# Kernel tuning notes

Measured on AMD Instinct MI355X. Metric: run time of the kernel, lower is better.

Reference implementation:

```python
import jax, jax.numpy as jnp
import numpy as np

B, S, D_MODEL, H = 2, 2048, 768, 12
HD = D_MODEL // H  # head_dim = 64
EPS = 1e-5


def setup_inputs() -> dict:
    key = jax.random.key(0)
    ks = jax.random.split(key, 5)
    sc = 0.02
    return {
        "x": jax.random.normal(ks[0], (B, S, D_MODEL), dtype=jnp.float32),
        "Wproj_w": jax.random.normal(ks[1], (7 * D_MODEL, D_MODEL), dtype=jnp.float32) * sc,
        "Wproj_b": jax.random.normal(ks[2], (7 * D_MODEL,), dtype=jnp.float32) * sc,
        "gn_w": jnp.ones((D_MODEL,), dtype=jnp.float32),
        "gn_b": jnp.zeros((D_MODEL,), dtype=jnp.float32),
        "out_w": jax.random.normal(ks[3], (D_MODEL, D_MODEL), dtype=jnp.float32) * sc,
        "out_b": jax.random.normal(ks[4], (D_MODEL,), dtype=jnp.float32) * sc,
    }


def _time_swiglu(qkv):
    # qkv: [B, S, 7, H, D]
    q1, k1, q2, k2, q3, k3, v = [qkv[:, :, i] for i in range(7)]
    a1 = jnp.einsum('bthd,bshd->bhts', q1, k1)  # [B,H,S,S], raw scores, no softmax
    a2 = jnp.einsum('bthd,bshd->bhts', q2, k2)
    a3 = jnp.einsum('bthd,bshd->bhts', q3, k3)
    t1 = jax.nn.silu(jnp.einsum('bhts,bshd->bthd', a1, v))
    t2 = jnp.einsum('bhts,bshd->bthd', a2, v)
    return jnp.einsum('bhts,bshd->bthd', a3, t1 * t2)  # [B,S,H,D]


def _group_norm(ctx, gn_w, gn_b):
    # ctx: [B, S, D_MODEL]; torch applies GroupNorm(H, D_MODEL) over (B, C=D_MODEL, L=S)
    g = ctx.reshape(B, S, H, HD)
    mean = jnp.mean(g, axis=(1, 3), keepdims=True)          # per (batch, group) over (S, HD)
    var = jnp.var(g, axis=(1, 3), keepdims=True)
    g = (g - mean) * jax.lax.rsqrt(var + EPS)
    g = g.reshape(B, S, D_MODEL)
    return g * gn_w + gn_b


def reference(x, Wproj_w, Wproj_b, gn_w, gn_b, out_w, out_b):
    qkv = x @ Wproj_w.T + Wproj_b                  # [B,S,7*D_MODEL]
    qkv = qkv.reshape(B, S, 7, H, HD)
    ctx = _time_swiglu(qkv).reshape(B, S, D_MODEL)  # [B,S,D_MODEL]
    ctx = _group_norm(ctx, gn_w, gn_b)
    return ctx @ out_w.T + out_b
```

## Files before the change

kernel.cpp:

```cpp
#include <hip/hip_runtime.h>
#include <hip/hip_bf16.h>
#include <stdint.h>

typedef short short8 __attribute__((ext_vector_type(8)));
typedef float f32x4 __attribute__((ext_vector_type(4)));
typedef float f32x16 __attribute__((ext_vector_type(16)));
typedef unsigned short u16x4 __attribute__((ext_vector_type(4)));
typedef unsigned uint4v __attribute__((ext_vector_type(4)));

#define MFMA16 __builtin_amdgcn_mfma_f32_16x16x32_bf16
#define MFMA32 __builtin_amdgcn_mfma_f32_32x32x16_bf16

typedef unsigned int __attribute__((address_space(1))) as1_u32;
typedef unsigned int __attribute__((address_space(3))) as3_u32;
#define GLOAD16(gsrc, ldst) \
  __builtin_amdgcn_global_load_lds((const as1_u32*)(gsrc), (as3_u32*)(ldst), 16, 0, 0)

__device__ __forceinline__ unsigned short f2bf(float f) {
  __hip_bfloat16 h = __float2bfloat16(f);
  return *(unsigned short*)&h;
}
__device__ __forceinline__ unsigned pk2(float lo, float hi) {
  return ((unsigned)f2bf(hi) << 16) | (unsigned)f2bf(lo);
}
__device__ __forceinline__ void plswap(unsigned &a, unsigned &b) {
  asm volatile("v_permlane32_swap_b32 %0, %1" : "+v"(a), "+v"(b));
}

__device__ __forceinline__ short8 pv_frag(const f32x16* acc, int kc2) {
  int n = kc2 >> 1, c = kc2 & 1;
  int o0 = 2 * c, o1 = 2 * c + 1;
  unsigned x0 = pk2(acc[n][o0 * 4 + 0], acc[n][o0 * 4 + 1]);
  unsigned x1 = pk2(acc[n][o0 * 4 + 2], acc[n][o0 * 4 + 3]);
  unsigned y0 = pk2(acc[n][o1 * 4 + 0], acc[n][o1 * 4 + 1]);
  unsigned y1 = pk2(acc[n][o1 * 4 + 2], acc[n][o1 * 4 + 3]);
  plswap(x0, y0);
  plswap(x1, y1);
  uint4v fu; fu.x = x0; fu.y = x1; fu.z = y0; fu.w = y1;
  return __builtin_bit_cast(short8, fu);
}

__global__ __launch_bounds__(256) void cvt_bf16_4(const float* __restrict__ in,
                                                  unsigned short* __restrict__ out,
                                                  int n) {
  int i = (blockIdx.x * 256 + threadIdx.x) * 4;
  if (i >= n) return;
  f32x4 v = *(const f32x4*)(in + i);
  u16x4 o;
  o.x = f2bf(v.x); o.y = f2bf(v.y); o.z = f2bf(v.z); o.w = f2bf(v.w);
  *(u16x4*)(out + i) = o;
}

__global__ __launch_bounds__(256) void transp64(const unsigned short* __restrict__ src,
                                                int stride, int off,
                                                unsigned short* __restrict__ dst) {
  __shared__ __align__(16) unsigned short t[64 * 64];
  const int tid = threadIdx.x;
  const int tt = blockIdx.x, bh = blockIdx.y;
  const int b = bh / 12, h = bh % 12;
  const unsigned short* sbase = src + (size_t)(b * 2048 + tt * 64) * stride + h * 64 + off;
  for (int it = 0; it < 2; ++it) {
    int slot = it * 256 + tid, s = slot >> 3, j = slot & 7;
    short8 v = *(const short8*)(sbase + (size_t)s * stride + j * 8);
    int phys = (s + 8 * j) & 63;
    for (int e = 0; e < 8; ++e)
      t[(j * 8 + e) * 64 + phys] = ((unsigned short*)&v)[e];
  }
  __syncthreads();
  unsigned short* dbase = dst + (size_t)bh * 64 * 2048 + tt * 64;
  for (int it = 0; it < 2; ++it) {
    int slot = it * 256 + tid, d = slot >> 3, c = slot & 7;
    int pc = (c + (d >> 3)) & 7;
    short8 v = *(const short8*)(t + d * 64 + pc * 8);
    *(short8*)(dbase + (size_t)d * 2048 + c * 8) = v;
  }
}

template <bool OUT_BF16>
__global__ __launch_bounds__(256) void gemm_nt(const unsigned short* __restrict__ A,
                                               const unsigned short* __restrict__ Bm,
                                               const float* __restrict__ bias,
                                               void* __restrict__ Cout,
                                               int M, int N, int K) {
  __shared__ __align__(16) char smem[32768];
  char* As = smem;
  char* Bs = smem + 16384;
  const int tid = threadIdx.x;
  const int w = tid >> 6, l = tid & 63;
  const int wm = w >> 1, wn = w & 1;
  const int gx = gridDim.x;
  const int lin = blockIdx.y * gx + blockIdx.x;
  const int cpx = (gx * gridDim.y) >> 3;
  const int swz = (lin & 7) * cpx + (lin >> 3);
  const int Row0 = (swz / gx) * 128, Col0 = (swz % gx) * 128;

  f32x4 z; z.x = 0.f; z.y = 0.f; z.z = 0.f; z.w = 0.f;
  f32x4 acc[4][4];
  for (int m = 0; m < 4; ++m)
    for (int n = 0; n < 4; ++n) acc[m][n] = z;

  for (int k0 = 0; k0 < K; k0 += 64) {
    for (int it = 0; it < 4; ++it) {
      int slot = it * 256 + tid;
      int row = slot >> 3, j = slot & 7;
      int gc = j ^ (row & 7);
      GLOAD16(A + (size_t)(Row0 + row) * K + k0 + gc * 8, As + slot * 16);
      GLOAD16(Bm + (size_t)(Col0 + row) * K + k0 + gc * 8, Bs + slot * 16);
    }
    __syncthreads();
    for (int kc = 0; kc < 2; ++kc) {
      int c = (l >> 4) + 4 * kc;
      short8 af[4], bf[4];
      for (int m = 0; m < 4; ++m) {
        int t = wm * 64 + m * 16 + (l & 15);
        af[m] = *(const short8*)(As + t * 128 + ((c ^ (t & 7)) * 16));
      }
      for (int n = 0; n < 4; ++n) {
        int t = wn * 64 + n * 16 + (l & 15);
        bf[n] = *(const short8*)(Bs + t * 128 + ((c ^ (t & 7)) * 16));
      }
      for (int m = 0; m < 4; ++m)
        for (int n = 0; n < 4; ++n)
          acc[m][n] = MFMA16(af[m], bf[n], acc[m][n], 0, 0, 0);
    }
    __syncthreads();
  }
  for (int n = 0; n < 4; ++n) {
    int col = Col0 + wn * 64 + n * 16 + (l & 15);
    float bv = bias[col];
    for (int m = 0; m < 4; ++m) {
      int rbase = Row0 + wm * 64 + m * 16 + (l >> 4) * 4;
      for (int r = 0; r < 4; ++r) {
        float v = acc[m][n][r] + bv;
        size_t idx = (size_t)(rbase + r) * N + col;
        if (OUT_BF16) ((unsigned short*)Cout)[idx] = f2bf(v);
        else          ((float*)Cout)[idx] = v;
      }
    }
  }
}

__global__ __launch_bounds__(256) void pass1(const unsigned short* __restrict__ qkv,
                                             const unsigned short* __restrict__ vt,
                                             unsigned short* __restrict__ u) {
  __shared__ __align__(16) char smem[49152];
  const int tid = threadIdx.x, w = tid >> 6, l = tid & 63;
  const int m = w & 1, sh = w >> 1;
  const int g5 = l >> 5, l31 = l & 31;
  const int tt = blockIdx.x, bh = blockIdx.y;
  const int b = bh / 12, h = bh % 12;

  short8 qf[2][4];
#pragma unroll
  for (int tb = 0; tb < 2; ++tb) {
    const unsigned short* qrow =
        qkv + (size_t)(b * 2048 + tt * 64 + tb * 32 + l31) * 5376 + h * 64 + m * 2 * 768;
#pragma unroll
    for (int kc = 0; kc < 4; ++kc)
      qf[tb][kc] = *(const short8*)(qrow + kc * 16 + g5 * 8);
  }

  f32x16 z16;
#pragma unroll
  for (int i = 0; i < 16; ++i) z16[i] = 0.f;
  f32x16 tacc[2][2];
  tacc[0][0] = z16; tacc[0][1] = z16; tacc[1][0] = z16; tacc[1][1] = z16;

  auto STAGE = [&](char* buf, int si) {
#pragma unroll
    for (int shs = 0; shs < 2; ++shs) {
      int s0 = shs * 1024 + si * 32;
      char* hb = buf + shs * 12288;
      {
        int row = tid >> 3, pc = tid & 7, gc = pc ^ (row & 7);
        const unsigned short* base =
            qkv + (size_t)(b * 2048 + s0 + row) * 5376 + h * 64 + gc * 8;
        GLOAD16(base + 768, hb + tid * 16);
        GLOAD16(base + 3 * 768, hb + 4096 + tid * 16);
      }
      {
        int row = tid >> 2, pc = tid & 3, gc = pc ^ ((row >> 1) & 3);
        GLOAD16(vt + (size_t)(bh * 64 + row) * 2048 + s0 + gc * 8,
                hb + 8192 + tid * 16);
      }
    }
  };

  STAGE(smem, 0);
  __syncthreads();
  for (int si = 0; si < 32; ++si) {
    const char* cur = smem + (si & 1) * 24576 + sh * 12288;
    if (si < 31) STAGE(smem + ((si + 1) & 1) * 24576, si + 1);
    const char* Ks = cur + m * 4096;
    const char* Vs = cur + 8192;

    short8 kreg[4], vreg[4];
#pragma unroll
    for (int kc = 0; kc < 4; ++kc)
      kreg[kc] = *(const short8*)(Ks + l31 * 128 + (((kc * 2 + g5) ^ (l31 & 7)) * 16));
#pragma unroll
    for (int kc2 = 0; kc2 < 2; ++kc2)
#pragma unroll
      for (int dn = 0; dn < 2; ++dn) {
        int drow = dn * 32 + l31, c = kc2 * 2 + g5;
        vreg[kc2 * 2 + dn] =
            *(const short8*)(Vs + drow * 64 + ((c ^ ((drow >> 1) & 3)) * 16));
      }

#pragma unroll
    for (int tb = 0; tb < 2; ++tb) {
      f32x16 a = z16;
#pragma unroll
      for (int kc = 0; kc < 4; ++kc)
        a = MFMA32(kreg[kc], qf[tb][kc], a, 0, 0, 0);
#pragma unroll
      for (int kc2 = 0; kc2 < 2; ++kc2) {
        short8 pa = pv_frag(&a, kc2);
#pragma unroll
        for (int dn = 0; dn < 2; ++dn)
          tacc[tb][dn] = MFMA32(pa, vreg[kc2 * 2 + dn], tacc[tb][dn], 0, 0, 0);
      }
    }
    __syncthreads();
  }

  float* ex = (float*)smem;
  if (sh == 1) {
#pragma unroll
    for (int tb = 0; tb < 2; ++tb)
#pragma unroll
      for (int dn = 0; dn < 2; ++dn)
#pragma unroll
        for (int qd = 0; qd < 4; ++qd) {
          f32x4 v;
          v.x = tacc[tb][dn][qd * 4 + 0]; v.y = tacc[tb][dn][qd * 4 + 1];
          v.z = tacc[tb][dn][qd * 4 + 2]; v.w = tacc[tb][dn][qd * 4 + 3];
          *(f32x4*)((char*)ex + m * 16384 + ((tb * 2 + dn) * 4 + qd) * 1024 + l * 16) = v;
        }
  }
  __syncthreads();
  if (sh == 0) {
#pragma unroll
    for (int tb = 0; tb < 2; ++tb)
#pragma unroll
      for (int dn = 0; dn < 2; ++dn)
#pragma unroll
        for (int qd = 0; qd < 4; ++qd) {
          f32x4 v = *(const f32x4*)((char*)ex + m * 16384 +
                                    ((tb * 2 + dn) * 4 + qd) * 1024 + l * 16);
          tacc[tb][dn][qd * 4 + 0] += v.x; tacc[tb][dn][qd * 4 + 1] += v.y;
          tacc[tb][dn][qd * 4 + 2] += v.z; tacc[tb][dn][qd * 4 + 3] += v.w;
        }
  }
  __syncthreads();
  if (sh == 0 && m == 1) {
#pragma unroll
    for (int tb = 0; tb < 2; ++tb)
#pragma unroll
      for (int dn = 0; dn < 2; ++dn)
#pragma unroll
        for (int qd = 0; qd < 4; ++qd) {
          f32x4 v;
          v.x = tacc[tb][dn][qd * 4 + 0]; v.y = tacc[tb][dn][qd * 4 + 1];
          v.z = tacc[tb][dn][qd * 4 + 2]; v.w = tacc[tb][dn][qd * 4 + 3];
          *(f32x4*)((char*)ex + ((tb * 2 + dn) * 4 + qd) * 1024 + l * 16) = v;
        }
  }
  __syncthreads();
  if (sh == 0 && m == 0) {
#pragma unroll
    for (int tb = 0; tb < 2; ++tb)
#pragma unroll
      for (int dn = 0; dn < 2; ++dn)
#pragma unroll
        for (int r = 0; r < 16; ++r) {
          float x2 = ex[((tb * 2 + dn) * 4 + (r >> 2)) * 256 + l * 4 + (r & 3)];
          int crow = (r & 3) + 8 * (r >> 2) + 4 * g5;
          int t = tt * 64 + tb * 32 + crow;
          int d = dn * 32 + l31;
          float x1 = tacc[tb][dn][r];
          float uu = (x1 / (1.f + expf(-x1))) * x2;
          u[(size_t)(b * 2048 + t) * 768 + h * 64 + d] = f2bf(uu);
        }
  }
}

__global__ __launch_bounds__(256) void pass2(const unsigned short* __restrict__ qkv,
                                             const unsigned short* __restrict__ ut,
                                             float* __restrict__ ctx,
                                             float* __restrict__ partials) {
  __shared__ __align__(16) char smem[65536];
  const int tid = threadIdx.x, w = tid >> 6, l = tid & 63;
  const int g5 = l >> 5, l31 = l & 31;
  const int tt = blockIdx.x, bh = blockIdx.y;
  const int b = bh / 12, h = bh % 12;

  short8 qf[2][4];
#pragma unroll
  for (int tb = 0; tb < 2; ++tb) {
    const unsigned short* qrow =
        qkv + (size_t)(b * 2048 + tt * 64 + tb * 32 + l31) * 5376 + h * 64 + 4 * 768;
#pragma unroll
    for (int kc = 0; kc < 4; ++kc)
      qf[tb][kc] = *(const short8*)(qrow + kc * 16 + g5 * 8);
  }

  f32x16 z16;
#pragma unroll
  for (int i = 0; i < 16; ++i) z16[i] = 0.f;
  f32x16 ca[2][2];
  ca[0][0] = z16; ca[0][1] = z16; ca[1][0] = z16; ca[1][1] = z16;

  const unsigned short *kp0, *kp1, *kp2, *kp3, *up0, *up1, *up2, *up3;
  {
    int row = tid >> 3, pc = tid & 7, gc = pc ^ (row & 7);
    kp0 = qkv + (size_t)(b * 2048 + row) * 5376 + h * 64 + 5 * 768 + gc * 8;
    kp1 = kp0 + (size_t)512 * 5376;
    kp2 = kp1 + (size_t)512 * 5376;
    kp3 = kp2 + (size_t)512 * 5376;
    int rowv = tid >> 2, pcv = tid & 3, gcv = pcv ^ ((rowv >> 1) & 3);
    up0 = ut + (size_t)(bh * 64 + rowv) * 2048 + gcv * 8;
    up1 = up0 + 512; up2 = up1 + 512; up3 = up2 + 512;
  }
  auto STAGE = [&](char* buf) {
    GLOAD16(kp0, buf + tid * 16);
    GLOAD16(up0, buf + 4096 + tid * 16);
    GLOAD16(kp1, buf + 8192 + tid * 16);
    GLOAD16(up1, buf + 12288 + tid * 16);
    GLOAD16(kp2, buf + 16384 + tid * 16);
    GLOAD16(up2, buf + 20480 + tid * 16);
    GLOAD16(kp3, buf + 24576 + tid * 16);
    GLOAD16(up3, buf + 28672 + tid * 16);
    kp0 += 32 * 5376; kp1 += 32 * 5376; kp2 += 32 * 5376; kp3 += 32 * 5376;
    up0 += 32; up1 += 32; up2 += 32; up3 += 32;
  };

  STAGE(smem);
  __syncthreads();
  for (int si = 0; si < 16; ++si) {
    const char* cur = smem + (si & 1) * 32768;
    if (si < 15) STAGE(smem + ((si + 1) & 1) * 32768);
    const char* Ks = cur + w * 8192;
    const char* Us = Ks + 4096;

    short8 kreg[4], ureg[4];
#pragma unroll
    for (int kc = 0; kc < 4; ++kc)
      kreg[kc] = *(const short8*)(Ks + l31 * 128 + (((kc * 2 + g5) ^ (l31 & 7)) * 16));
#pragma unroll
    for (int kc2 = 0; kc2 < 2; ++kc2)
#pragma unroll
      for (int dn = 0; dn < 2; ++dn) {
        int drow = dn * 32 + l31, c = kc2 * 2 + g5;
        ureg[kc2 * 2 + dn] =
            *(const short8*)(Us + drow * 64 + ((c ^ ((drow >> 1) & 3)) * 16));
      }

#pragma unroll
    for (int tb = 0; tb < 2; ++tb) {
      f32x16 a = z16;
#pragma unroll
      for (int kc = 0; kc < 4; ++kc)
        a = MFMA32(kreg[kc], qf[tb][kc], a, 0, 0, 0);
#pragma unroll
      for (int kc2 = 0; kc2 < 2; ++kc2) {
        short8 pa = pv_frag(&a, kc2);
#pragma unroll
        for (int dn = 0; dn < 2; ++dn)
          ca[tb][dn] = MFMA32(pa, ureg[kc2 * 2 + dn], ca[tb][dn], 0, 0, 0);
      }
    }
    __syncthreads();
  }

  float* ex = (float*)smem;
  auto DUMP = [&](int region) {
#pragma unroll
    for (int tb = 0; tb < 2; ++tb)
#pragma unroll
      for (int dn = 0; dn < 2; ++dn)
#pragma unroll
        for (int qd = 0; qd < 4; ++qd) {
          f32x4 v;
          v.x = ca[tb][dn][qd * 4 + 0]; v.y = ca[tb][dn][qd * 4 + 1];
          v.z = ca[tb][dn][qd * 4 + 2]; v.w = ca[tb][dn][qd * 4 + 3];
          *(f32x4*)((char*)ex + region * 16384 + ((tb * 2 + dn) * 4 + qd) * 1024 + l * 16) = v;
        }
  };
  auto ACCUM = [&](int region) {
#pragma unroll
    for (int tb = 0; tb < 2; ++tb)
#pragma unroll
      for (int dn = 0; dn < 2; ++dn)
#pragma unroll
        for (int qd = 0; qd < 4; ++qd) {
          f32x4 v = *(const f32x4*)((char*)ex + region * 16384 +
                                    ((tb * 2 + dn) * 4 + qd) * 1024 + l * 16);
          ca[tb][dn][qd * 4 + 0] += v.x; ca[tb][dn][qd * 4 + 1] += v.y;
          ca[tb][dn][qd * 4 + 2] += v.z; ca[tb][dn][qd * 4 + 3] += v.w;
        }
  };
  if (w == 1) DUMP(0);
  if (w == 3) DUMP(1);
  __syncthreads();
  if (w == 0) ACCUM(0);
  if (w == 2) ACCUM(1);
  __syncthreads();
  if (w == 2) DUMP(0);
  __syncthreads();
  float psum = 0.f, psum2 = 0.f;
  if (w == 0) {
    ACCUM(0);
#pragma unroll
    for (int tb = 0; tb < 2; ++tb)
#pragma unroll
      for (int dn = 0; dn < 2; ++dn)
#pragma unroll
        for (int r = 0; r < 16; ++r) {
          int t = tt * 64 + tb * 32 + (r & 3) + 8 * (r >> 2) + 4 * g5;
          int d = dn * 32 + l31;
          float v = ca[tb][dn][r];
          ctx[(size_t)(b * 2048 + t) * 768 + h * 64 + d] = v;
          psum += v; psum2 += v * v;
        }
    for (int off = 32; off > 0; off >>= 1) {
      psum += __shfl_down(psum, off, 64);
      psum2 += __shfl_down(psum2, off, 64);
    }
    if (l == 0) {
      partials[(bh * 32 + tt) * 2] = psum;
      partials[(bh * 32 + tt) * 2 + 1] = psum2;
    }
  }
}

__global__ __launch_bounds__(64) void gn_finalize(const float* __restrict__ partials,
                                                  float* __restrict__ stats) {
  const int g = blockIdx.x;
  const int l = threadIdx.x;
  double s = 0.0, s2 = 0.0;
  if (l < 32) {
    s = (double)partials[(g * 32 + l) * 2];
    s2 = (double)partials[(g * 32 + l) * 2 + 1];
  }
  for (int off = 32; off > 0; off >>= 1) {
    s += __shfl_down(s, off, 64);
    s2 += __shfl_down(s2, off, 64);
  }
  if (l == 0) {
    const double N = 2048.0 * 64.0;
    double mean = s / N;
    double var = s2 / N - mean * mean;
    stats[g * 2] = (float)mean;
    stats[g * 2 + 1] = (float)(1.0 / sqrt(var + 1e-5));
  }
}

__global__ __launch_bounds__(256) void gn_apply(const float* __restrict__ ctx,
                                                const float* __restrict__ stats,
                                                const float* __restrict__ gw,
                                                const float* __restrict__ gb,
                                                unsigned short* __restrict__ outc) {
  int i = blockIdx.x * 256 + threadIdx.x;
  if (i >= 4096 * 768) return;
  int c = i % 768;
  int b = i / (2048 * 768);
  int g = b * 12 + (c >> 6);
  float v = (ctx[i] - stats[2 * g]) * stats[2 * g + 1];
  outc[i] = f2bf(v * gw[c] + gb[c]);
}

extern "C" void kernel_launch(void* const* d_in, const int* in_sizes, int n_in,
                              void* d_out, int out_size, void* d_ws, size_t ws_size,
                              hipStream_t stream) {
  const float* x   = (const float*)d_in[0];
  const float* Wpw = (const float*)d_in[1];
  const float* Wpb = (const float*)d_in[2];
  const float* gnw = (const float*)d_in[3];
  const float* gnb = (const float*)d_in[4];
  const float* ow  = (const float*)d_in[5];
  const float* ob  = (const float*)d_in[6];
  float* out = (float*)d_out;

  char* ws = (char*)d_ws;
  size_t off = 0;
  auto carve = [&](size_t bytes) {
    char* p = ws + off;
    off = (off + bytes + 255) & ~(size_t)255;
    return p;
  };
  unsigned short* xb   = (unsigned short*)carve((size_t)4096 * 768 * 2);
  unsigned short* wb   = (unsigned short*)carve((size_t)5376 * 768 * 2);
  unsigned short* owb  = (unsigned short*)carve((size_t)768 * 768 * 2);
  unsigned short* qkvb = (unsigned short*)carve((size_t)4096 * 5376 * 2);
  unsigned short* ub   = (unsigned short*)carve((size_t)4096 * 768 * 2);
  unsigned short* vtb  = (unsigned short*)carve((size_t)24 * 64 * 2048 * 2);
  unsigned short* utb  = (unsigned short*)carve((size_t)24 * 64 * 2048 * 2);
  float* ctx           = (float*)carve((size_t)4096 * 768 * 4);
  float* partials      = (float*)carve(24 * 32 * 2 * 4);
  float* stats         = (float*)carve(48 * 4);

  cvt_bf16_4<<<3072, 256, 0, stream>>>(x, xb, 4096 * 768);
  cvt_bf16_4<<<4032, 256, 0, stream>>>(Wpw, wb, 5376 * 768);
  cvt_bf16_4<<<576, 256, 0, stream>>>(ow, owb, 768 * 768);

  gemm_nt<true><<<dim3(42, 32), 256, 0, stream>>>(xb, wb, Wpb, qkvb, 4096, 5376, 768);
  transp64<<<dim3(32, 24), 256, 0, stream>>>(qkvb, 5376, 6 * 768, vtb);
  pass1<<<dim3(32, 24), 256, 0, stream>>>(qkvb, vtb, ub);
  transp64<<<dim3(32, 24), 256, 0, stream>>>(ub, 768, 0, utb);
  pass2<<<dim3(32, 24), 256, 0, stream>>>(qkvb, utb, ctx, partials);
  gn_finalize<<<24, 64, 0, stream>>>(partials, stats);
  gn_apply<<<12288, 256, 0, stream>>>(ctx, stats, gnw, gnb, xb);
  gemm_nt<false><<<dim3(6, 32), 256, 0, stream>>>(xb, owb, ob, out, 4096, 768, 768);
}
```

Before: 220.8 us.

## Widen pass1 blocks to 128 query rows sharing staged K/V tiles

pass1 now runs 512-thread blocks that each cover 128 query rows (two 64-row halves) over half as many blocks, so each staged K1/K2/V tile in shared memory serves twice as many queries. Staging work is split between the two thread halves and the cross-wave reduction runs in two phases to fit the existing shared buffer. The intent is to halve global and LDS staging traffic per query. The cost is extra barriers in the epilogue, a grid of only 384 blocks, and a (512,2) launch bound that may limit registers.

```diff
diff --git a/kernel.cpp b/kernel.cpp
--- a/kernel.cpp
+++ b/kernel.cpp
@@ -140,12 +140,13 @@
   }
 }
 
-__global__ __launch_bounds__(256) void pass1(const unsigned short* __restrict__ qkv,
-                                             const unsigned short* __restrict__ vt,
-                                             unsigned short* __restrict__ u) {
+__global__ __launch_bounds__(512, 2) void pass1(const unsigned short* __restrict__ qkv,
+                                                const unsigned short* __restrict__ vt,
+                                                unsigned short* __restrict__ u) {
   __shared__ __align__(16) char smem[49152];
   const int tid = threadIdx.x, w = tid >> 6, l = tid & 63;
-  const int m = w & 1, sh = w >> 1;
+  const int m = w & 1, th = (w >> 1) & 1, sh = w >> 2;
+  const int tidh = tid & 255, ths = tid >> 8;
   const int g5 = l >> 5, l31 = l & 31;
   const int tt = blockIdx.x, bh = blockIdx.y;
   const int b = bh / 12, h = bh % 12;
@@ -154,7 +155,8 @@
 #pragma unroll
   for (int tb = 0; tb < 2; ++tb) {
     const unsigned short* qrow =
-        qkv + (size_t)(b * 2048 + tt * 64 + tb * 32 + l31) * 5376 + h * 64 + m * 2 * 768;
+        qkv + (size_t)(b * 2048 + tt * 128 + th * 64 + tb * 32 + l31) * 5376 +
+        h * 64 + m * 1536;
 #pragma unroll
     for (int kc = 0; kc < 4; ++kc)
       qf[tb][kc] = *(const short8*)(qrow + kc * 16 + g5 * 8);
@@ -167,22 +169,19 @@
   tacc[0][0] = z16; tacc[0][1] = z16; tacc[1][0] = z16; tacc[1][1] = z16;
 
   auto STAGE = [&](char* buf, int si) {
-#pragma unroll
-    for (int shs = 0; shs < 2; ++shs) {
-      int s0 = shs * 1024 + si * 32;
-      char* hb = buf + shs * 12288;
-      {
-        int row = tid >> 3, pc = tid & 7, gc = pc ^ (row & 7);
-        const unsigned short* base =
-            qkv + (size_t)(b * 2048 + s0 + row) * 5376 + h * 64 + gc * 8;
-        GLOAD16(base + 768, hb + tid * 16);
-        GLOAD16(base + 3 * 768, hb + 4096 + tid * 16);
-      }
-      {
-        int row = tid >> 2, pc = tid & 3, gc = pc ^ ((row >> 1) & 3);
-        GLOAD16(vt + (size_t)(bh * 64 + row) * 2048 + s0 + gc * 8,
-                hb + 8192 + tid * 16);
-      }
+    int s0 = ths * 1024 + si * 32;
+    char* hb = buf + ths * 12288;
+    {
+      int row = tidh >> 3, pc = tidh & 7, gc = pc ^ (row & 7);
+      const unsigned short* base =
+          qkv + (size_t)(b * 2048 + s0 + row) * 5376 + h * 64 + gc * 8;
+      GLOAD16(base + 768, hb + tidh * 16);
+      GLOAD16(base + 3 * 768, hb + 4096 + tidh * 16);
+    }
+    {
+      int row = tidh >> 2, pc = tidh & 3, gc = pc ^ ((row >> 1) & 3);
+      GLOAD16(vt + (size_t)(bh * 64 + row) * 2048 + s0 + gc * 8,
+              hb + 8192 + tidh * 16);
     }
   };
 
@@ -225,63 +224,67 @@
   }
 
   float* ex = (float*)smem;
-  if (sh == 1) {
-#pragma unroll
-    for (int tb = 0; tb < 2; ++tb)
-#pragma unroll
-      for (int dn = 0; dn < 2; ++dn)
-#pragma unroll
-        for (int qd = 0; qd < 4; ++qd) {
-          f32x4 v;
-          v.x = tacc[tb][dn][qd * 4 + 0]; v.y = tacc[tb][dn][qd * 4 + 1];
-          v.z = tacc[tb][dn][qd * 4 + 2]; v.w = tacc[tb][dn][qd * 4 + 3];
-          *(f32x4*)((char*)ex + m * 16384 + ((tb * 2 + dn) * 4 + qd) * 1024 + l * 16) = v;
-        }
-  }
-  __syncthreads();
-  if (sh == 0) {
-#pragma unroll
-    for (int tb = 0; tb < 2; ++tb)
-#pragma unroll
-      for (int dn = 0; dn < 2; ++dn)
-#pragma unroll
-        for (int qd = 0; qd < 4; ++qd) {
-          f32x4 v = *(const f32x4*)((char*)ex + m * 16384 +
-                                    ((tb * 2 + dn) * 4 + qd) * 1024 + l * 16);
-          tacc[tb][dn][qd * 4 + 0] += v.x; tacc[tb][dn][qd * 4 + 1] += v.y;
-          tacc[tb][dn][qd * 4 + 2] += v.z; tacc[tb][dn][qd * 4 + 3] += v.w;
-        }
-  }
-  __syncthreads();
-  if (sh == 0 && m == 1) {
-#pragma unroll
-    for (int tb = 0; tb < 2; ++tb)
-#pragma unroll
-      for (int dn = 0; dn < 2; ++dn)
-#pragma unroll
-        for (int qd = 0; qd < 4; ++qd) {
-          f32x4 v;
-          v.x = tacc[tb][dn][qd * 4 + 0]; v.y = tacc[tb][dn][qd * 4 + 1];
-          v.z = tacc[tb][dn][qd * 4 + 2]; v.w = tacc[tb][dn][qd * 4 + 3];
-          *(f32x4*)((char*)ex + ((tb * 2 + dn) * 4 + qd) * 1024 + l * 16) = v;
-        }
-  }
-  __syncthreads();
-  if (sh == 0 && m == 0) {
-#pragma unroll
-    for (int tb = 0; tb < 2; ++tb)
-#pragma unroll
-      for (int dn = 0; dn < 2; ++dn)
-#pragma unroll
-        for (int r = 0; r < 16; ++r) {
-          float x2 = ex[((tb * 2 + dn) * 4 + (r >> 2)) * 256 + l * 4 + (r & 3)];
-          int crow = (r & 3) + 8 * (r >> 2) + 4 * g5;
-          int t = tt * 64 + tb * 32 + crow;
-          int d = dn * 32 + l31;
-          float x1 = tacc[tb][dn][r];
-          float uu = (x1 / (1.f + expf(-x1))) * x2;
-          u[(size_t)(b * 2048 + t) * 768 + h * 64 + d] = f2bf(uu);
-        }
+#pragma unroll 1
+  for (int ph = 0; ph < 2; ++ph) {
+    if (sh == 1 && th == ph) {
+#pragma unroll
+      for (int tb = 0; tb < 2; ++tb)
+#pragma unroll
+        for (int dn = 0; dn < 2; ++dn)
+#pragma unroll
+          for (int qd = 0; qd < 4; ++qd) {
+            f32x4 v;
+            v.x = tacc[tb][dn][qd * 4 + 0]; v.y = tacc[tb][dn][qd * 4 + 1];
+            v.z = tacc[tb][dn][qd * 4 + 2]; v.w = tacc[tb][dn][qd * 4 + 3];
+            *(f32x4*)((char*)ex + m * 16384 + ((tb * 2 + dn) * 4 + qd) * 1024 + l * 16) = v;
+          }
+    }
+    __syncthreads();
+    if (sh == 0 && th == ph) {
+#pragma unroll
+      for (int tb = 0; tb < 2; ++tb)
+#pragma unroll
+        for (int dn = 0; dn < 2; ++dn)
+#pragma unroll
+          for (int qd = 0; qd < 4; ++qd) {
+            f32x4 v = *(const f32x4*)((char*)ex + m * 16384 +
+                                      ((tb * 2 + dn) * 4 + qd) * 1024 + l * 16);
+            tacc[tb][dn][qd * 4 + 0] += v.x; tacc[tb][dn][qd * 4 + 1] += v.y;
+            tacc[tb][dn][qd * 4 + 2] += v.z; tacc[tb][dn][qd * 4 + 3] += v.w;
+          }
+    }
+    __syncthreads();
+    if (sh == 0 && th == ph && m == 1) {
+#pragma unroll
+      for (int tb = 0; tb < 2; ++tb)
+#pragma unroll
+        for (int dn = 0; dn < 2; ++dn)
+#pragma unroll
+          for (int qd = 0; qd < 4; ++qd) {
+            f32x4 v;
+            v.x = tacc[tb][dn][qd * 4 + 0]; v.y = tacc[tb][dn][qd * 4 + 1];
+            v.z = tacc[tb][dn][qd * 4 + 2]; v.w = tacc[tb][dn][qd * 4 + 3];
+            *(f32x4*)((char*)ex + ((tb * 2 + dn) * 4 + qd) * 1024 + l * 16) = v;
+          }
+    }
+    __syncthreads();
+    if (sh == 0 && th == ph && m == 0) {
+#pragma unroll
+      for (int tb = 0; tb < 2; ++tb)
+#pragma unroll
+        for (int dn = 0; dn < 2; ++dn)
+#pragma unroll
+          for (int r = 0; r < 16; ++r) {
+            float x2 = ex[((tb * 2 + dn) * 4 + (r >> 2)) * 256 + l * 4 + (r & 3)];
+            int crow = (r & 3) + 8 * (r >> 2) + 4 * g5;
+            int t = tt * 128 + th * 64 + tb * 32 + crow;
+            int d = dn * 32 + l31;
+            float x1 = tacc[tb][dn][r];
+            float uu = (x1 / (1.f + expf(-x1))) * x2;
+            u[(size_t)(b * 2048 + t) * 768 + h * 64 + d] = f2bf(uu);
+          }
+    }
+    __syncthreads();
   }
 }
 
@@ -506,7 +509,7 @@
 
   gemm_nt<true><<<dim3(42, 32), 256, 0, stream>>>(xb, wb, Wpb, qkvb, 4096, 5376, 768);
   transp64<<<dim3(32, 24), 256, 0, stream>>>(qkvb, 5376, 6 * 768, vtb);
-  pass1<<<dim3(32, 24), 256, 0, stream>>>(qkvb, vtb, ub);
+  pass1<<<dim3(16, 24), 512, 0, stream>>>(qkvb, vtb, ub);
   transp64<<<dim3(32, 24), 256, 0, stream>>>(ub, 768, 0, utb);
   pass2<<<dim3(32, 24), 256, 0, stream>>>(qkvb, utb, ctx, partials);
   gn_finalize<<<24, 64, 0, stream>>>(partials, stats);
```

New measurement: 227.5 us. +3.0%, slower.
